# Kernel optimization log

Measured on AMD Instinct MI355X. Metric: run time of the kernel, lower is better.

## Reference

```python
import jax, jax.numpy as jnp
import numpy as np

EPS = 1e-16


def setup_inputs() -> dict:
    key = jax.random.key(0)
    k1, k2 = jax.random.split(key)
    N, D = 512, 4096
    a = jax.random.normal(k1, (N, D), dtype=jnp.float32)
    p = jax.random.normal(k2, (N, D), dtype=jnp.float32)
    return {"a": a, "p": p}


def reference(a, p):
    N = a.shape[0]
    # Pairwise squared distances between anchors a and positives p:
    # ||a_i||^2 - 2 a_i . p_j + ||p_j||^2   (diag(a a^T) == row norms)
    dot = jnp.matmul(a, p.T)                       # [N, N]
    sq_a = jnp.sum(a * a, axis=-1)                 # [N]
    sq_p = jnp.sum(p * p, axis=-1)                 # [N]
    d2 = sq_a[:, None] - 2.0 * dot + sq_p[None, :]
    d2 = jnp.maximum(d2, 0.0)                      # distances[distances < 0] = 0
    zero_mask = (d2 == 0.0).astype(d2.dtype)
    dist = (1.0 - zero_mask) * jnp.sqrt(d2 + zero_mask * EPS)  # [N, N]

    # Triplet tensor: loss[a, p, n] = dist[a, p] - dist[a, n]
    triplet = dist[:, :, None] - dist[:, None, :]  # [N, N, N]

    # Validity mask: labels = arange(N) -> valid iff p == anchor and n != anchor
    labels = jnp.arange(N)
    label_eq = labels[:, None] == labels[None, :]  # [N, N]
    mask = label_eq[:, :, None] & (~label_eq[:, None, :])  # [N, N, N]

    triplet = mask.astype(triplet.dtype) * triplet
    triplet = jax.nn.relu(triplet)

    num_positive = jnp.sum(triplet > EPS).astype(triplet.dtype)
    loss = jnp.sum(triplet) / (num_positive + EPS)
    return loss
```

## Files before the change

kernel.cpp:

```cpp
#include <hip/hip_runtime.h>
#include <math.h>

#define PN 512
#define PD 4096

#define F_SA 0
#define F_SP 512
#define F_DD 1024
#define F_SUM 1536
#define F_CNT 1537
#define F_DONE 1538
#define WS_AH_BYTES 8192
#define WS_PH_BYTES (8192 + 4194304)
#define WS_NEED ((size_t)(8192 + 2 * 4194304))

typedef __attribute__((ext_vector_type(8))) short short8;
typedef __attribute__((ext_vector_type(4))) float floatx4;

static __device__ __forceinline__ unsigned short f2bf(float x) {
    unsigned int u = __float_as_uint(x);
    u += 0x7fffu + ((u >> 16) & 1u);
    return (unsigned short)(u >> 16);
}

static __device__ __forceinline__ void load16_lds(const void* gp, void* lp) {
    __builtin_amdgcn_global_load_lds(
        (const __attribute__((address_space(1))) unsigned int*)gp,
        (__attribute__((address_space(3))) unsigned int*)lp,
        16, 0, 0);
}

struct ushort4s { unsigned short x, y, z, w; };

__global__ __launch_bounds__(256) void taw_prep_kernel(
        const float* __restrict__ a, const float* __restrict__ p,
        float* __restrict__ ws) {
    const int i = blockIdx.x;
    const int t = threadIdx.x;
    if (i == 0 && t < 64) ((unsigned int*)ws)[1536 + t] = 0u;
    const float4* a4 = (const float4*)(a + (size_t)i * PD);
    const float4* p4 = (const float4*)(p + (size_t)i * PD);
    unsigned short* ah = (unsigned short*)((char*)ws + WS_AH_BYTES) + (size_t)i * PD;
    unsigned short* ph = (unsigned short*)((char*)ws + WS_PH_BYTES) + (size_t)i * PD;
    float sa = 0.f, sp = 0.f, dp = 0.f;
#pragma unroll
    for (int c = 0; c < 4; ++c) {
        const int e = c * 256 + t;
        float4 av = a4[e];
        float4 pv = p4[e];
        sa += av.x * av.x + av.y * av.y + av.z * av.z + av.w * av.w;
        sp += pv.x * pv.x + pv.y * pv.y + pv.z * pv.z + pv.w * pv.w;
        dp += av.x * pv.x + av.y * pv.y + av.z * pv.z + av.w * pv.w;
        ushort4s ab = {f2bf(av.x), f2bf(av.y), f2bf(av.z), f2bf(av.w)};
        ushort4s pb = {f2bf(pv.x), f2bf(pv.y), f2bf(pv.z), f2bf(pv.w)};
        *(ushort4s*)(ah + (size_t)e * 4) = ab;
        *(ushort4s*)(ph + (size_t)e * 4) = pb;
    }
#pragma unroll
    for (int off = 32; off > 0; off >>= 1) {
        sa += __shfl_down(sa, off, 64);
        sp += __shfl_down(sp, off, 64);
        dp += __shfl_down(dp, off, 64);
    }
    __shared__ float red[3][4];
    const int wave = t >> 6;
    if ((t & 63) == 0) { red[0][wave] = sa; red[1][wave] = sp; red[2][wave] = dp; }
    __syncthreads();
    if (t == 0) {
        sa = red[0][0] + red[0][1] + red[0][2] + red[0][3];
        sp = red[1][0] + red[1][1] + red[1][2] + red[1][3];
        dp = red[2][0] + red[2][1] + red[2][2] + red[2][3];
        float d2 = sa - 2.f * dp + sp;
        d2 = fmaxf(d2, 0.f);
        ws[F_SA + i] = sa;
        ws[F_SP + i] = sp;
        ws[F_DD + i] = (d2 == 0.f) ? 0.f : sqrtf(d2);
    }
}

__global__ __launch_bounds__(1024) void taw_fused_kernel(float* __restrict__ ws,
                                                         float* __restrict__ out) {
    __shared__ __attribute__((aligned(16))) char shraw[32768];
    short* sbase = (short*)shraw;
    float* rbase = (float*)shraw;
    const unsigned short* ah = (const unsigned short*)((const char*)ws + WS_AH_BYTES);
    const unsigned short* ph = (const unsigned short*)((const char*)ws + WS_PH_BYTES);
    unsigned int* wsu = (unsigned int*)ws;

    const int t = threadIdx.x;
    const int lane = t & 63;
    const int w = t >> 6;
    const int kg = w >> 2;
    const int quad = w & 3;
    const int qm = quad >> 1, qn = quad & 1;
    const int i0 = blockIdx.y * 32;
    const int j0 = blockIdx.x * 32;
    const int kgbase = kg << 10;

#define SG_OFF(KG, ARR, G) (((((KG) * 2 + (ARR)) * 4) + (G)) * 512)

    const int lrow = ((quad & 1) << 4) + (lane & 15);
    const int lkof = ((quad >> 1) << 5) + ((lane >> 4) << 3);
    const unsigned short* agp = ah + (size_t)(i0 + lrow) * PD + kgbase + lkof;
    const unsigned short* pgp = ph + (size_t)(j0 + lrow) * PD + kgbase + lkof;
    short* sA = sbase + SG_OFF(kg, 0, quad);
    short* sB = sbase + SG_OFF(kg, 1, quad);

    floatx4 acc = {0.f, 0.f, 0.f, 0.f};
    const int lane8 = lane * 8;

    for (int st = 0; st < 16; ++st) {
        __syncthreads();
        load16_lds(agp + st * 64, sA);
        load16_lds(pgp + st * 64, sB);
        __syncthreads();
        short8 af0 = *(const short8*)(sbase + SG_OFF(kg, 0, qm) + lane8);
        short8 bf0 = *(const short8*)(sbase + SG_OFF(kg, 1, qn) + lane8);
        short8 af1 = *(const short8*)(sbase + SG_OFF(kg, 0, 2 + qm) + lane8);
        short8 bf1 = *(const short8*)(sbase + SG_OFF(kg, 1, 2 + qn) + lane8);
        acc = __builtin_amdgcn_mfma_f32_16x16x32_bf16(af0, bf0, acc, 0, 0, 0);
        acc = __builtin_amdgcn_mfma_f32_16x16x32_bf16(af1, bf1, acc, 0, 0, 0);
    }

    __syncthreads();
    *(floatx4*)(rbase + (((kg * 4 + quad) * 64) + lane) * 4) = acc;
    __syncthreads();

    __shared__ float rs[4];
    __shared__ unsigned int rc[4];
    if (kg == 0) {
        floatx4 d = *(const floatx4*)(rbase + (((0 * 4 + quad) * 64) + lane) * 4);
#pragma unroll
        for (int k = 1; k < 4; ++k)
            d += *(const floatx4*)(rbase + (((k * 4 + quad) * 64) + lane) * 4);
        const int gj = j0 + qn * 16 + (lane & 15);
        const float spj = ws[F_SP + gj];
        float lsum = 0.f;
        unsigned int lcnt = 0;
#pragma unroll
        for (int r = 0; r < 4; ++r) {
            const int gi = i0 + qm * 16 + ((lane >> 4) << 2) + r;
            float d2 = ws[F_SA + gi] - 2.f * d[r] + spj;
            d2 = fmaxf(d2, 0.f);
            const float dist = (d2 == 0.f) ? 0.f : sqrtf(d2);
            const float v = (gi != gj) ? fmaxf(ws[F_DD + gi] - dist, 0.f) : 0.f;
            lsum += v;
            lcnt += (v > 1e-16f) ? 1u : 0u;
        }
#pragma unroll
        for (int off = 32; off > 0; off >>= 1) {
            lsum += __shfl_down(lsum, off, 64);
            lcnt += __shfl_down(lcnt, off, 64);
        }
        if (lane == 0) { rs[quad] = lsum; rc[quad] = lcnt; }
    }
    __syncthreads();
    if (t == 0) {
        atomicAdd(ws + F_SUM, rs[0] + rs[1] + rs[2] + rs[3]);
        atomicAdd(&wsu[F_CNT], rc[0] + rc[1] + rc[2] + rc[3]);
        __threadfence();
        if (atomicAdd(&wsu[F_DONE], 1u) == 255u) {
            __threadfence();
            const float s = atomicAdd(ws + F_SUM, 0.0f);
            const unsigned int c = atomicAdd(&wsu[F_CNT], 0u);
            out[0] = (float)((double)s / ((double)c + 1e-16));
        }
    }
#undef SG_OFF
}

__global__ __launch_bounds__(256) void taw_gemm_loss_kernel(
        const float* __restrict__ A, const float* __restrict__ P,
        float* __restrict__ ws) {
    __shared__ float as[32][34];
    __shared__ float bs[32][34];
    const int tx = threadIdx.x;
    const int ty = threadIdx.y;
    const int t = ty * 16 + tx;
    const int i0 = blockIdx.y * 32;
    const int j0 = blockIdx.x * 32;
    const int sr = t >> 3;
    const int sk = (t & 7) * 4;
    const float* aptr = A + (size_t)(i0 + sr) * PD + sk;
    const float* pptr = P + (size_t)(j0 + sr) * PD + sk;
    float c00 = 0.f, c01 = 0.f, c10 = 0.f, c11 = 0.f;
    for (int k0 = 0; k0 < PD; k0 += 32) {
        float4 av = *(const float4*)(aptr + k0);
        float4 pv = *(const float4*)(pptr + k0);
        __syncthreads();
        as[sk + 0][sr] = av.x; as[sk + 1][sr] = av.y;
        as[sk + 2][sr] = av.z; as[sk + 3][sr] = av.w;
        bs[sk + 0][sr] = pv.x; bs[sk + 1][sr] = pv.y;
        bs[sk + 2][sr] = pv.z; bs[sk + 3][sr] = pv.w;
        __syncthreads();
#pragma unroll
        for (int kk = 0; kk < 32; ++kk) {
            const float2 a2 = *(const float2*)&as[kk][2 * ty];
            const float2 b2 = *(const float2*)&bs[kk][2 * tx];
            c00 = fmaf(a2.x, b2.x, c00);
            c01 = fmaf(a2.x, b2.y, c01);
            c10 = fmaf(a2.y, b2.x, c10);
            c11 = fmaf(a2.y, b2.y, c11);
        }
    }
    const int i = i0 + 2 * ty;
    const int j = j0 + 2 * tx;
    float cvals[2][2] = {{c00, c01}, {c10, c11}};
    float lsum = 0.f;
    unsigned int lcnt = 0;
#pragma unroll
    for (int dr = 0; dr < 2; ++dr)
#pragma unroll
        for (int dc = 0; dc < 2; ++dc) {
            const int ii = i + dr, jj = j + dc;
            float d2 = ws[F_SA + ii] - 2.f * cvals[dr][dc] + ws[F_SP + jj];
            d2 = fmaxf(d2, 0.f);
            const float dist = (d2 == 0.f) ? 0.f : sqrtf(d2);
            const float v = (ii != jj) ? fmaxf(ws[F_DD + ii] - dist, 0.f) : 0.f;
            lsum += v;
            lcnt += (v > 1e-16f) ? 1u : 0u;
        }
#pragma unroll
    for (int off = 32; off > 0; off >>= 1) {
        lsum += __shfl_down(lsum, off, 64);
        lcnt += __shfl_down(lcnt, off, 64);
    }
    __shared__ float rsum[4];
    __shared__ unsigned int rcnt[4];
    if ((t & 63) == 0) { rsum[t >> 6] = lsum; rcnt[t >> 6] = lcnt; }
    __syncthreads();
    if (t == 0) {
        atomicAdd(ws + F_SUM, rsum[0] + rsum[1] + rsum[2] + rsum[3]);
        atomicAdd(((unsigned int*)ws) + F_CNT, rcnt[0] + rcnt[1] + rcnt[2] + rcnt[3]);
    }
}

__global__ void taw_finalize_kernel(const float* __restrict__ ws,
                                    float* __restrict__ out) {
    const double s = (double)ws[F_SUM];
    const double c = (double)(((const unsigned int*)ws)[F_CNT]);
    out[0] = (float)(s / (c + 1e-16));
}

extern "C" void kernel_launch(void* const* d_in, const int* in_sizes, int n_in,
                              void* d_out, int out_size, void* d_ws, size_t ws_size,
                              hipStream_t stream) {
    (void)in_sizes; (void)n_in; (void)out_size;
    const float* a = (const float*)d_in[0];
    const float* p = (const float*)d_in[1];
    float* out = (float*)d_out;
    float* ws = (float*)d_ws;

    taw_prep_kernel<<<PN, 256, 0, stream>>>(a, p, ws);
    if (ws_size >= WS_NEED) {
        taw_fused_kernel<<<dim3(16, 16), 1024, 0, stream>>>(ws, out);
    } else {
        taw_gemm_loss_kernel<<<dim3(16, 16), dim3(16, 16), 0, stream>>>(a, p, ws);
        taw_finalize_kernel<<<1, 1, 0, stream>>>(ws, out);
    }
}
```

Measured before the change: 98.52 us.

## Double-buffer LDS tiles and halve K-split in fused distance GEMM

Restructures the fused bf16 MFMA GEMM kernel to use 512 threads with a 2-way K split instead of 4, larger 128-wide K stages, and a double-buffered LDS so the next stage's global-to-LDS loads are issued before the current stage's MFMAs. This drops one barrier per iteration and shrinks the cross-group reduction to a single add. It also removes the threadfences around the completion counter and replaces them with an artificial data dependence on the earlier atomic results. That ordering trick may be weaker than a real fence, and halving the threads per block reduces parallelism per tile.

```diff
diff --git a/kernel.cpp b/kernel.cpp
--- a/kernel.cpp
+++ b/kernel.cpp
@@ -3,6 +3,10 @@
 
 #define PN 512
 #define PD 4096
+
+#define NKG 2
+#define BKST 128
+#define NST (PD / NKG / BKST)
 
 #define F_SA 0
 #define F_SP 512
@@ -78,11 +82,9 @@
     }
 }
 
-__global__ __launch_bounds__(1024) void taw_fused_kernel(float* __restrict__ ws,
-                                                         float* __restrict__ out) {
-    __shared__ __attribute__((aligned(16))) char shraw[32768];
-    short* sbase = (short*)shraw;
-    float* rbase = (float*)shraw;
+__global__ __launch_bounds__(512) void taw_fused_kernel(float* __restrict__ ws,
+                                                        float* __restrict__ out) {
+    __shared__ short lds[2][NKG][2][8][64][8];
     const unsigned short* ah = (const unsigned short*)((const char*)ws + WS_AH_BYTES);
     const unsigned short* ph = (const unsigned short*)((const char*)ws + WS_PH_BYTES);
     unsigned int* wsu = (unsigned int*)ws;
@@ -91,48 +93,53 @@
     const int lane = t & 63;
     const int w = t >> 6;
     const int kg = w >> 2;
-    const int quad = w & 3;
-    const int qm = quad >> 1, qn = quad & 1;
+    const int q = w & 3;
+    const int qm = q >> 1, qn = q & 1;
     const int i0 = blockIdx.y * 32;
     const int j0 = blockIdx.x * 32;
-    const int kgbase = kg << 10;
-
-#define SG_OFF(KG, ARR, G) (((((KG) * 2 + (ARR)) * 4) + (G)) * 512)
-
-    const int lrow = ((quad & 1) << 4) + (lane & 15);
-    const int lkof = ((quad >> 1) << 5) + ((lane >> 4) << 3);
-    const unsigned short* agp = ah + (size_t)(i0 + lrow) * PD + kgbase + lkof;
-    const unsigned short* pgp = ph + (size_t)(j0 + lrow) * PD + kgbase + lkof;
-    short* sA = sbase + SG_OFF(kg, 0, quad);
-    short* sB = sbase + SG_OFF(kg, 1, quad);
+    const int kgbase = kg * (PD / NKG);
+
+    const int koff = kgbase + q * 32 + ((lane >> 4) << 3);
+    const unsigned short* agp0 = ah + (size_t)(i0 + (lane & 15)) * PD + koff;
+    const unsigned short* agp1 = ah + (size_t)(i0 + 16 + (lane & 15)) * PD + koff;
+    const unsigned short* pgp0 = ph + (size_t)(j0 + (lane & 15)) * PD + koff;
+    const unsigned short* pgp1 = ph + (size_t)(j0 + 16 + (lane & 15)) * PD + koff;
 
     floatx4 acc = {0.f, 0.f, 0.f, 0.f};
-    const int lane8 = lane * 8;
-
-    for (int st = 0; st < 16; ++st) {
+    int buf = 0;
+
+    load16_lds(agp0, &lds[0][kg][0][2 * q + 0][0][0]);
+    load16_lds(agp1, &lds[0][kg][0][2 * q + 1][0][0]);
+    load16_lds(pgp0, &lds[0][kg][1][2 * q + 0][0][0]);
+    load16_lds(pgp1, &lds[0][kg][1][2 * q + 1][0][0]);
+
+    for (int st = 0; st < NST; ++st) {
         __syncthreads();
-        load16_lds(agp + st * 64, sA);
-        load16_lds(pgp + st * 64, sB);
-        __syncthreads();
-        short8 af0 = *(const short8*)(sbase + SG_OFF(kg, 0, qm) + lane8);
-        short8 bf0 = *(const short8*)(sbase + SG_OFF(kg, 1, qn) + lane8);
-        short8 af1 = *(const short8*)(sbase + SG_OFF(kg, 0, 2 + qm) + lane8);
-        short8 bf1 = *(const short8*)(sbase + SG_OFF(kg, 1, 2 + qn) + lane8);
-        acc = __builtin_amdgcn_mfma_f32_16x16x32_bf16(af0, bf0, acc, 0, 0, 0);
-        acc = __builtin_amdgcn_mfma_f32_16x16x32_bf16(af1, bf1, acc, 0, 0, 0);
-    }
-
-    __syncthreads();
-    *(floatx4*)(rbase + (((kg * 4 + quad) * 64) + lane) * 4) = acc;
+        if (st + 1 < NST) {
+            const int kb = (st + 1) * BKST;
+            load16_lds(agp0 + kb, &lds[buf ^ 1][kg][0][2 * q + 0][0][0]);
+            load16_lds(agp1 + kb, &lds[buf ^ 1][kg][0][2 * q + 1][0][0]);
+            load16_lds(pgp0 + kb, &lds[buf ^ 1][kg][1][2 * q + 0][0][0]);
+            load16_lds(pgp1 + kb, &lds[buf ^ 1][kg][1][2 * q + 1][0][0]);
+        }
+#pragma unroll
+        for (int s = 0; s < 4; ++s) {
+            short8 af = *(const short8*)&lds[buf][kg][0][s * 2 + qm][lane][0];
+            short8 bf = *(const short8*)&lds[buf][kg][1][s * 2 + qn][lane][0];
+            acc = __builtin_amdgcn_mfma_f32_16x16x32_bf16(af, bf, acc, 0, 0, 0);
+        }
+        buf ^= 1;
+    }
+
+    __syncthreads();
+    float* fred = (float*)&lds[0][0][0][0][0][0];
+    if (kg == 1) *(floatx4*)(fred + (q * 64 + lane) * 4) = acc;
     __syncthreads();
 
     __shared__ float rs[4];
     __shared__ unsigned int rc[4];
     if (kg == 0) {
-        floatx4 d = *(const floatx4*)(rbase + (((0 * 4 + quad) * 64) + lane) * 4);
-#pragma unroll
-        for (int k = 1; k < 4; ++k)
-            d += *(const floatx4*)(rbase + (((k * 4 + quad) * 64) + lane) * 4);
+        acc += *(const floatx4*)(fred + (q * 64 + lane) * 4);
         const int gj = j0 + qn * 16 + (lane & 15);
         const float spj = ws[F_SP + gj];
         float lsum = 0.f;
@@ -140,7 +147,7 @@
 #pragma unroll
         for (int r = 0; r < 4; ++r) {
             const int gi = i0 + qm * 16 + ((lane >> 4) << 2) + r;
-            float d2 = ws[F_SA + gi] - 2.f * d[r] + spj;
+            float d2 = ws[F_SA + gi] - 2.f * acc[r] + spj;
             d2 = fmaxf(d2, 0.f);
             const float dist = (d2 == 0.f) ? 0.f : sqrtf(d2);
             const float v = (gi != gj) ? fmaxf(ws[F_DD + gi] - dist, 0.f) : 0.f;
@@ -152,21 +159,20 @@
             lsum += __shfl_down(lsum, off, 64);
             lcnt += __shfl_down(lcnt, off, 64);
         }
-        if (lane == 0) { rs[quad] = lsum; rc[quad] = lcnt; }
+        if (lane == 0) { rs[q] = lsum; rc[q] = lcnt; }
     }
     __syncthreads();
     if (t == 0) {
-        atomicAdd(ws + F_SUM, rs[0] + rs[1] + rs[2] + rs[3]);
-        atomicAdd(&wsu[F_CNT], rc[0] + rc[1] + rc[2] + rc[3]);
-        __threadfence();
-        if (atomicAdd(&wsu[F_DONE], 1u) == 255u) {
-            __threadfence();
+        const float oldsum = atomicAdd(ws + F_SUM, rs[0] + rs[1] + rs[2] + rs[3]);
+        const unsigned int oldcnt = atomicAdd(&wsu[F_CNT], rc[0] + rc[1] + rc[2] + rc[3]);
+        unsigned int dep = __float_as_uint(oldsum) | oldcnt;
+        asm volatile("" : "+v"(dep));
+        if (atomicAdd(&wsu[F_DONE], 1u + (dep & 0u)) == 255u) {
             const float s = atomicAdd(ws + F_SUM, 0.0f);
             const unsigned int c = atomicAdd(&wsu[F_CNT], 0u);
             out[0] = (float)((double)s / ((double)c + 1e-16));
         }
     }
-#undef SG_OFF
 }
 
 __global__ __launch_bounds__(256) void taw_gemm_loss_kernel(
@@ -253,7 +259,7 @@
 
     taw_prep_kernel<<<PN, 256, 0, stream>>>(a, p, ws);
     if (ws_size >= WS_NEED) {
-        taw_fused_kernel<<<dim3(16, 16), 1024, 0, stream>>>(ws, out);
+        taw_fused_kernel<<<dim3(16, 16), 512, 0, stream>>>(ws, out);
     } else {
         taw_gemm_loss_kernel<<<dim3(16, 16), dim3(16, 16), 0, stream>>>(a, p, ws);
         taw_finalize_kernel<<<1, 1, 0, stream>>>(ws, out);
```

Result: no change. 98.11 us (-0.4%).
